# Kernel optimization log

Hardware: AMD Instinct MI355X
Metric: run time of the kernel (lower is better)

The kernel has to match this reference:

```python
import jax, jax.numpy as jnp
import numpy as np

T, B_SZ = 1024, 1024
NX, NU, ND, NM, NDT, NH = 128, 64, 32, 32, 32, 128


def setup_inputs() -> dict:
    key = jax.random.key(0)
    ks = jax.random.split(key, 10)
    return {
        "x": jax.random.normal(ks[0], (B_SZ, NX), jnp.float32),
        "M_flow": jax.random.normal(ks[1], (T, B_SZ, NM), jnp.float32),
        "DT": jax.random.normal(ks[2], (T, B_SZ, NDT), jnp.float32),
        "D": jax.random.normal(ks[3], (T, B_SZ, ND), jnp.float32),
        # ConstrainedLinear(nx, nx): weight and scalar init with torch.rand -> uniform[0,1)
        "A_weight": jax.random.uniform(ks[4], (NX, NX), jnp.float32),
        "A_scalar": jax.random.uniform(ks[5], (NX, NX), jnp.float32),
        # nn.Linear(in, out, bias=False) weights are [out, in]
        "B_w": jax.random.normal(ks[6], (NX, NU), jnp.float32) * (1.0 / np.sqrt(NU)),
        "E_w": jax.random.normal(ks[7], (NX, ND), jnp.float32) * (1.0 / np.sqrt(ND)),
        "hf1_w": jax.random.normal(ks[8], (NH, NM + NDT), jnp.float32) * (1.0 / np.sqrt(NM + NDT)),
        "hf2_w": jax.random.normal(ks[9], (NU, NH), jnp.float32) * (1.0 / np.sqrt(NH)),
    }


def reference(x, M_flow, DT, D, A_weight, A_scalar, B_w, E_w, hf1_w, hf2_w):
    # Constrained weight: ((1 - 0.1*sigmoid(scalar)) * softmax(weight, dim=1)).T
    # It is constant across time, so compute once (torch redundantly recomputes it per step).
    s_clamped = 1.0 - 0.1 * jax.nn.sigmoid(A_scalar)
    W_eff = (s_clamped * jax.nn.softmax(A_weight, axis=1)).T  # [nx, nx]

    # Per-step control input u_t depends only on exogenous M_flow/DT -> vectorize over time.
    md = jnp.concatenate([M_flow, DT], axis=2)                # [T, B, n_m+n_dT]
    h = jax.nn.relu(jnp.einsum('tbi,hi->tbh', md, hf1_w))     # [T, B, n_hidden]
    u = jax.nn.relu(jnp.einsum('tbh,uh->tbu', h, hf2_w))      # [T, B, nu]

    # Precompute additive drive B(u_t) + E(d_t); only x@W_eff is sequential.
    drive = jnp.einsum('tbu,xu->tbx', u, B_w) + jnp.einsum('tbd,xd->tbx', D, E_w)

    def step(x_prev, drive_t):
        x_new = x_prev @ W_eff + drive_t
        return x_new, x_new

    _, X = jax.lax.scan(step, x, drive)  # X: [T, B, nx]
    Y = X[:, :, -1]                      # [T, B]
    return X, Y
```

## Files before the change

### kernel.cpp

```cpp
#include <hip/hip_runtime.h>

typedef _Float16 h4 __attribute__((ext_vector_type(4)));
typedef _Float16 h8 __attribute__((ext_vector_type(8)));
typedef float f4 __attribute__((ext_vector_type(4)));

#define MFMA16(a, b, c) __builtin_amdgcn_mfma_f32_16x16x32_f16((a), (b), (c), 0, 0, 0)

static constexpr int TT  = 1024;
static constexpr int BS  = 1024;
static constexpr int LCH = 32;
static constexpr int NCH = 32;
static constexpr size_t XTOT = (size_t)TT * BS * 128;

static constexpr size_t WS_WT16 = 0;
static constexpr size_t WS_HF1  = 32768;
static constexpr size_t WS_HF2  = 49152;
static constexpr size_t WS_BW   = 65536;
static constexpr size_t WS_EW   = 81920;
static constexpr size_t WS_W32  = 90112;
static constexpr size_t WS_F    = 131072;
static constexpr size_t WS_INIT = WS_F + (size_t)NCH * BS * 128 * 4;
static constexpr size_t WS_DRV  = WS_INIT + (size_t)NCH * BS * 128 * 4;

template <typename T>
__device__ inline T ntload(const T* p) { return __builtin_nontemporal_load(p); }

__global__ void prep_kernel(const float* __restrict__ Aw, const float* __restrict__ As,
                            const float* __restrict__ hf1, const float* __restrict__ hf2,
                            const float* __restrict__ Bw, const float* __restrict__ Ew,
                            char* __restrict__ ws)
{
    const int tid = threadIdx.x;
    const int bid = blockIdx.x;
    if (bid < 128) {
        __shared__ float red[128];
        const int n = bid;
        const float a = Aw[n * 128 + tid];
        red[tid] = a;
        __syncthreads();
        for (int s = 64; s > 0; s >>= 1) {
            if (tid < s) red[tid] = fmaxf(red[tid], red[tid + s]);
            __syncthreads();
        }
        const float mx = red[0];
        __syncthreads();
        const float e = expf(a - mx);
        red[tid] = e;
        __syncthreads();
        for (int s = 64; s > 0; s >>= 1) {
            if (tid < s) red[tid] += red[tid + s];
            __syncthreads();
        }
        const float sm  = e / red[0];
        const float asv = As[n * 128 + tid];
        const float sc  = 1.0f - 0.1f * (1.0f / (1.0f + expf(-asv)));
        ((_Float16*)(ws + WS_WT16))[n * 128 + tid] = (_Float16)(sc * sm);
    } else {
        const int b2 = bid - 128;
        for (int i = b2 * 128 + tid; i < 8192; i += 32 * 128) {
            ((_Float16*)(ws + WS_HF1))[i] = (_Float16)hf1[i];
            ((_Float16*)(ws + WS_HF2))[i] = (_Float16)hf2[i];
            ((_Float16*)(ws + WS_BW))[i]  = (_Float16)Bw[i];
            if (i < 4096) ((_Float16*)(ws + WS_EW))[i] = (_Float16)Ew[i];
        }
    }
}

__global__ void w32_kernel(char* __restrict__ ws)
{
    const int tid  = threadIdx.x;
    const int lane = tid & 63;
    const int w    = tid >> 6;
    const int cl   = lane & 15;
    const int gq   = lane >> 4;

    __shared__ __align__(16) _Float16 Ta[128 * 128];
    __shared__ __align__(16) _Float16 Tb[128 * 128];

    const _Float16* Wt16 = (const _Float16*)(ws + WS_WT16);
    for (int i = tid; i < 2048; i += 256)
        *(h8*)&Ta[i * 8] = *(const h8*)&Wt16[i * 8];
    __syncthreads();

    for (int s = 0; s < 5; ++s) {
        const _Float16* src = (s & 1) ? Tb : Ta;
        _Float16* dst       = (s & 1) ? Ta : Tb;
        f4 acc[8][2];
#pragma unroll
        for (int mt = 0; mt < 8; ++mt)
#pragma unroll
            for (int nt = 0; nt < 2; ++nt) acc[mt][nt] = f4{};
#pragma unroll
        for (int kk = 0; kk < 4; ++kk) {
            h8 b0, b1;
#pragma unroll
            for (int j = 0; j < 8; ++j) {
                const int kr = kk * 32 + gq * 8 + j;
                b0[j] = src[kr * 128 + w * 32 + cl];
                b1[j] = src[kr * 128 + w * 32 + 16 + cl];
            }
#pragma unroll
            for (int mt = 0; mt < 8; ++mt) {
                h8 a = *(const h8*)&src[(mt * 16 + cl) * 128 + kk * 32 + gq * 8];
                acc[mt][0] = MFMA16(a, b0, acc[mt][0]);
                acc[mt][1] = MFMA16(a, b1, acc[mt][1]);
            }
        }
        __syncthreads();
#pragma unroll
        for (int mt = 0; mt < 8; ++mt)
#pragma unroll
            for (int nt = 0; nt < 2; ++nt)
#pragma unroll
                for (int r = 0; r < 4; ++r)
                    dst[(mt * 16 + gq * 4 + r) * 128 + w * 32 + nt * 16 + cl] =
                        (_Float16)acc[mt][nt][r];
        __syncthreads();
    }
    _Float16* W32 = (_Float16*)(ws + WS_W32);
    for (int i = tid; i < 2048; i += 256)
        *(h8*)&W32[i * 8] = *(const h8*)&Tb[i * 8];
}

__global__ __launch_bounds__(256, 4)
void drive_kernel(const float* __restrict__ Mfl, const float* __restrict__ DTi,
                  const float* __restrict__ Din, char* __restrict__ ws)
{
    const int tid  = threadIdx.x;
    const int lane = tid & 63;
    const int w    = tid >> 6;
    const int cl   = lane & 15;
    const int gq   = lane >> 4;
    const int bt   = blockIdx.x & 63;
    const int tq   = blockIdx.x >> 6;
    const int b0   = bt * 16;

    const _Float16* Hf1  = (const _Float16*)(ws + WS_HF1);
    const _Float16* Hf2  = (const _Float16*)(ws + WS_HF2);
    const _Float16* Bw16 = (const _Float16*)(ws + WS_BW);
    const _Float16* Ew16 = (const _Float16*)(ws + WS_EW);
    _Float16* Drv        = (_Float16*)(ws + WS_DRV);

    __shared__ __align__(16) _Float16 mds[4][16 * 64];
    __shared__ __align__(16) _Float16 dts[4][16 * 32];
    __shared__ __align__(16) _Float16 hs[4][16 * 128];
    __shared__ __align__(16) _Float16 us[4][16 * 64];

    const int qrow = (tid & 127) >> 3;
    const int qc4  = (tid & 7) * 4;
    f4 pm[4], pd[4];
#pragma unroll
    for (int s = 0; s < 4; ++s) {
        const size_t t  = (size_t)tq * 4 + s;
        const size_t rb = (t * BS + b0 + qrow) * 32 + qc4;
        pm[s] = (tid < 128) ? ntload((const f4*)&Mfl[rb]) : ntload((const f4*)&DTi[rb]);
        if (tid < 128) pd[s] = ntload((const f4*)&Din[rb]);
    }
#pragma unroll
    for (int s = 0; s < 4; ++s) {
        const int col = (tid < 128) ? qc4 : (32 + qc4);
        h4 hv;
#pragma unroll
        for (int j = 0; j < 4; ++j) hv[j] = (_Float16)pm[s][j];
        *(h4*)&mds[s][qrow * 64 + (((col >> 3) ^ (qrow & 7)) * 8) + (col & 7)] = hv;
        if (tid < 128) {
            h4 h2;
#pragma unroll
            for (int j = 0; j < 4; ++j) h2[j] = (_Float16)pd[s][j];
            *(h4*)&dts[s][qrow * 32 + (((qc4 >> 3) ^ (qrow & 3)) * 8) + (qc4 & 7)] = h2;
        }
    }

    h8 hf1f[2][2], bwf[2][2], ewf[2], hf2f[4];
#pragma unroll
    for (int nt = 0; nt < 2; ++nt) {
        const int ng = w * 32 + nt * 16 + cl;
#pragma unroll
        for (int kk = 0; kk < 2; ++kk) {
            hf1f[nt][kk] = *(const h8*)&Hf1[ng * 64 + kk * 32 + gq * 8];
            bwf[nt][kk]  = *(const h8*)&Bw16[ng * 64 + kk * 32 + gq * 8];
        }
        ewf[nt] = *(const h8*)&Ew16[ng * 32 + gq * 8];
    }
    {
        const int ng = w * 16 + cl;
#pragma unroll
        for (int kk = 0; kk < 4; ++kk)
            hf2f[kk] = *(const h8*)&Hf2[ng * 128 + kk * 32 + gq * 8];
    }
    __syncthreads();

#pragma unroll
    for (int s = 0; s < 4; ++s) {
        f4 ha[2] = {};
#pragma unroll
        for (int kk = 0; kk < 2; ++kk) {
            h8 a = *(const h8*)&mds[s][cl * 64 + (((kk * 4 + gq) ^ (cl & 7)) * 8)];
            ha[0] = MFMA16(hf1f[0][kk], a, ha[0]);
            ha[1] = MFMA16(hf1f[1][kk], a, ha[1]);
        }
#pragma unroll
        for (int nt = 0; nt < 2; ++nt) {
            const int nb8 = w * 4 + nt * 2 + (gq >> 1);
            h4 hv;
#pragma unroll
            for (int r = 0; r < 4; ++r) hv[r] = (_Float16)fmaxf(ha[nt][r], 0.f);
            *(h4*)&hs[s][cl * 128 + ((nb8 ^ cl) & 15) * 8 + (gq & 1) * 4] = hv;
        }
    }
    __syncthreads();

#pragma unroll
    for (int s = 0; s < 4; ++s) {
        f4 ua = {};
#pragma unroll
        for (int kt = 0; kt < 4; ++kt) {
            h8 a = *(const h8*)&hs[s][cl * 128 + (((kt * 4 + gq) ^ cl) & 15) * 8];
            ua = MFMA16(hf2f[kt], a, ua);
        }
        const int nb8 = w * 2 + (gq >> 1);
        h4 hv;
#pragma unroll
        for (int r = 0; r < 4; ++r) hv[r] = (_Float16)fmaxf(ua[r], 0.f);
        *(h4*)&us[s][cl * 64 + ((nb8 ^ (cl & 7)) & 7) * 8 + (gq & 1) * 4] = hv;
    }
    __syncthreads();

#pragma unroll
    for (int s = 0; s < 4; ++s) {
        f4 acc[2] = {};
#pragma unroll
        for (int kk = 0; kk < 2; ++kk) {
            h8 a = *(const h8*)&us[s][cl * 64 + (((kk * 4 + gq) ^ (cl & 7)) & 7) * 8];
            acc[0] = MFMA16(bwf[0][kk], a, acc[0]);
            acc[1] = MFMA16(bwf[1][kk], a, acc[1]);
        }
        {
            h8 a = *(const h8*)&dts[s][cl * 32 + ((gq ^ (cl & 3)) * 8)];
            acc[0] = MFMA16(ewf[0], a, acc[0]);
            acc[1] = MFMA16(ewf[1], a, acc[1]);
        }
        h8 o;
#pragma unroll
        for (int r = 0; r < 4; ++r) { o[r] = (_Float16)acc[0][r]; o[4 + r] = (_Float16)acc[1][r]; }
        const size_t t = (size_t)tq * 4 + s;
        *(h8*)&Drv[((t * 64 + bt) * 256 + tid) * 8] = o;
    }
}

template <bool FINAL>
__global__ __launch_bounds__(256, 2)
void scan_kernel(char* __restrict__ ws,
                 float* __restrict__ Xout, float* __restrict__ Yout)
{
    const int wslot = threadIdx.x >> 6;
    const int wid   = blockIdx.x * 4 + wslot;
    const int lane  = threadIdx.x & 63;
    const int cl = lane & 15, gq = lane >> 4;
    const int c  = wid >> 6;
    const int bt = wid & 63;
    const int b0 = bt * 16;

    const _Float16* Wt16 = (const _Float16*)(ws + WS_WT16);
    const _Float16* Drv  = (const _Float16*)(ws + WS_DRV);
    float* Fbuf       = (float*)(ws + WS_F);
    const float* Init = (const float*)(ws + WS_INIT);

    __shared__ __align__(16) _Float16 tb[4][16 * 128];
    _Float16* tbuf = tb[wslot];

    h8 wf[8][4];
#pragma unroll
    for (int nt = 0; nt < 8; ++nt)
#pragma unroll
        for (int kt = 0; kt < 4; ++kt)
            wf[nt][kt] = *(const h8*)&Wt16[(nt * 16 + cl) * 128 + kt * 32 + gq * 8];

    h8 xf[4];
    if constexpr (FINAL) {
        f4 iv[8];
#pragma unroll
        for (int nt = 0; nt < 8; ++nt)
            iv[nt] = *(const f4*)&Init[((size_t)c * BS + b0 + cl) * 128 + nt * 16 + gq * 4];
#pragma unroll
        for (int nt = 0; nt < 8; ++nt) {
            h4 hv;
#pragma unroll
            for (int r = 0; r < 4; ++r) hv[r] = (_Float16)iv[nt][r];
            *(h4*)&tbuf[cl * 128 + (((nt * 2 + (gq >> 1)) ^ cl) & 15) * 8 + (gq & 1) * 4] = hv;
        }
#pragma unroll
        for (int kt = 0; kt < 4; ++kt)
            xf[kt] = *(const h8*)&tbuf[cl * 128 + (((kt * 4 + gq) ^ cl) & 15) * 8];
    } else {
#pragma unroll
        for (int kt = 0; kt < 4; ++kt) xf[kt] = h8{};
    }

    constexpr size_t STEP = 16384;
    const h8* dp = (const h8*)Drv + (((size_t)(c * LCH) * 64 + bt) * 4) * 64 + lane;
    h8 dra0, dra1, dra2, dra3, drb0, drb1, drb2, drb3;
    dra0 = dp[0];          dra1 = dp[64];          dra2 = dp[128];          dra3 = dp[192];
    drb0 = dp[STEP];       drb1 = dp[STEP + 64];   drb2 = dp[STEP + 128];   drb3 = dp[STEP + 192];

#define SCAN_STEP(K, D0, D1, D2, D3)                                                     \
    {                                                                                    \
        f4 acc[8];                                                                       \
        _Pragma("unroll") for (int r = 0; r < 4; ++r) {                                  \
            acc[0][r] = (float)D0[r]; acc[1][r] = (float)D0[4 + r];                      \
            acc[2][r] = (float)D1[r]; acc[3][r] = (float)D1[4 + r];                      \
            acc[4][r] = (float)D2[r]; acc[5][r] = (float)D2[4 + r];                      \
            acc[6][r] = (float)D3[r]; acc[7][r] = (float)D3[4 + r];                      \
        }                                                                                \
        if ((K) + 2 < LCH) {                                                             \
            D0 = dp[(size_t)((K) + 2) * STEP + 0];                                       \
            D1 = dp[(size_t)((K) + 2) * STEP + 64];                                      \
            D2 = dp[(size_t)((K) + 2) * STEP + 128];                                     \
            D3 = dp[(size_t)((K) + 2) * STEP + 192];                                     \
        }                                                                                \
        _Pragma("unroll") for (int kt = 0; kt < 4; ++kt)                                 \
            _Pragma("unroll") for (int nt = 0; nt < 8; ++nt)                             \
                acc[nt] = MFMA16(wf[nt][kt], xf[kt], acc[nt]);                           \
        if constexpr (FINAL) {                                                           \
            const size_t t = (size_t)c * LCH + (K);                                      \
            float* xp = &Xout[(t * BS + b0 + cl) * 128 + gq * 4];                        \
            _Pragma("unroll") for (int nt = 0; nt < 8; ++nt)                             \
                __builtin_nontemporal_store(acc[nt], (f4*)&xp[nt * 16]);                 \
            if (gq == 3)                                                                 \
                __builtin_nontemporal_store(acc[7][3], &Yout[t * BS + b0 + cl]);         \
        } else if ((K) == LCH - 1) {                                                     \
            _Pragma("unroll") for (int nt = 0; nt < 8; ++nt)                             \
                *(f4*)&Fbuf[((size_t)c * BS + b0 + cl) * 128 + nt * 16 + gq * 4] =       \
                    acc[nt];                                                             \
        }                                                                                \
        if ((K) < LCH - 1) {                                                             \
            _Pragma("unroll") for (int nt = 0; nt < 8; ++nt) {                           \
                h4 hv;                                                                   \
                _Pragma("unroll") for (int r = 0; r < 4; ++r)                            \
                    hv[r] = (_Float16)acc[nt][r];                                        \
                *(h4*)&tbuf[cl * 128 + (((nt * 2 + (gq >> 1)) ^ cl) & 15) * 8 +          \
                            (gq & 1) * 4] = hv;                                          \
            }                                                                            \
            _Pragma("unroll") for (int kt = 0; kt < 4; ++kt)                             \
                xf[kt] = *(const h8*)&tbuf[cl * 128 + (((kt * 4 + gq) ^ cl) & 15) * 8];  \
        }                                                                                \
    }

    for (int k = 0; k < LCH; k += 2) {
        SCAN_STEP(k, dra0, dra1, dra2, dra3);
        SCAN_STEP(k + 1, drb0, drb1, drb2, drb3);
    }
#undef SCAN_STEP
}

__global__ __launch_bounds__(64, 1)
void carry_kernel(const float* __restrict__ x0, char* __restrict__ ws, int n_steps)
{
    const int lane = threadIdx.x;
    const int cl = lane & 15, gq = lane >> 4;
    const int b0 = blockIdx.x * 16;

    const _Float16* W32 = (const _Float16*)(ws + WS_W32);
    const float* Fbuf   = (const float*)(ws + WS_F);
    float* Init         = (float*)(ws + WS_INIT);

    __shared__ __align__(16) _Float16 tbuf[16 * 128];

    h8 wf[8][4];
#pragma unroll
    for (int nt = 0; nt < 8; ++nt)
#pragma unroll
        for (int kt = 0; kt < 4; ++kt)
            wf[nt][kt] = *(const h8*)&W32[(nt * 16 + cl) * 128 + kt * 32 + gq * 8];

    h8 xf[4];
    {
        f4 iv[8];
#pragma unroll
        for (int nt = 0; nt < 8; ++nt)
            iv[nt] = *(const f4*)&x0[(size_t)(b0 + cl) * 128 + nt * 16 + gq * 4];
#pragma unroll
        for (int nt = 0; nt < 8; ++nt)
            *(f4*)&Init[(size_t)(b0 + cl) * 128 + nt * 16 + gq * 4] = iv[nt];
#pragma unroll
        for (int nt = 0; nt < 8; ++nt) {
            h4 hv;
#pragma unroll
            for (int r = 0; r < 4; ++r) hv[r] = (_Float16)iv[nt][r];
            *(h4*)&tbuf[cl * 128 + (((nt * 2 + (gq >> 1)) ^ cl) & 15) * 8 + (gq & 1) * 4] = hv;
        }
#pragma unroll
        for (int kt = 0; kt < 4; ++kt)
            xf[kt] = *(const h8*)&tbuf[cl * 128 + (((kt * 4 + gq) ^ cl) & 15) * 8];
    }

    for (int cc = 1; cc <= n_steps; ++cc) {
        f4 acc[8];
#pragma unroll
        for (int nt = 0; nt < 8; ++nt)
            acc[nt] = *(const f4*)&Fbuf[((size_t)(cc - 1) * BS + b0 + cl) * 128 + nt * 16 + gq * 4];
#pragma unroll
        for (int kt = 0; kt < 4; ++kt)
#pragma unroll
            for (int nt = 0; nt < 8; ++nt)
                acc[nt] = MFMA16(wf[nt][kt], xf[kt], acc[nt]);
#pragma unroll
        for (int nt = 0; nt < 8; ++nt)
            *(f4*)&Init[((size_t)cc * BS + b0 + cl) * 128 + nt * 16 + gq * 4] = acc[nt];
        if (cc < n_steps) {
#pragma unroll
            for (int nt = 0; nt < 8; ++nt) {
                h4 hv;
#pragma unroll
                for (int r = 0; r < 4; ++r) hv[r] = (_Float16)acc[nt][r];
                *(h4*)&tbuf[cl * 128 + (((nt * 2 + (gq >> 1)) ^ cl) & 15) * 8 + (gq & 1) * 4] = hv;
            }
#pragma unroll
            for (int kt = 0; kt < 4; ++kt)
                xf[kt] = *(const h8*)&tbuf[cl * 128 + (((kt * 4 + gq) ^ cl) & 15) * 8];
        }
    }
}

extern "C" void kernel_launch(void* const* d_in, const int* in_sizes, int n_in,
                              void* d_out, int out_size, void* d_ws, size_t ws_size,
                              hipStream_t stream)
{
    const float* x_in = (const float*)d_in[0];
    const float* Mfl  = (const float*)d_in[1];
    const float* DTi  = (const float*)d_in[2];
    const float* Din  = (const float*)d_in[3];
    const float* Aw   = (const float*)d_in[4];
    const float* As   = (const float*)d_in[5];
    const float* Bw   = (const float*)d_in[6];
    const float* Ew   = (const float*)d_in[7];
    const float* hf1  = (const float*)d_in[8];
    const float* hf2  = (const float*)d_in[9];
    char* ws    = (char*)d_ws;
    float* Xout = (float*)d_out;
    float* Yout = Xout + XTOT;

    prep_kernel<<<dim3(160), dim3(128), 0, stream>>>(Aw, As, hf1, hf2, Bw, Ew, ws);
    w32_kernel<<<dim3(1), dim3(256), 0, stream>>>(ws);

    drive_kernel<<<dim3(256 * 64), dim3(256), 0, stream>>>(Mfl, DTi, Din, ws);
    scan_kernel<false><<<dim3(496), dim3(256), 0, stream>>>(ws, nullptr, nullptr);
    carry_kernel<<<dim3(64), dim3(64), 0, stream>>>(x_in, ws, 31);
    scan_kernel<true><<<dim3(512), dim3(256), 0, stream>>>(ws, Xout, Yout);
}
```

Baseline: 456.0 us.

## Fuse drive computation with local chunk scan and split pipeline into halves

Replaces the separate drive kernel and the non-final scan pass with a fused kernel that computes the MLP drive per step and immediately runs the zero-initialised local chunk scan, writing drive and chunk-end states. The timeline is split into two halves of 16 chunks, each with its own fused, carry and final-scan launches, so the drive buffer only needs to hold half the time range. The w32 matrix power kernel is also restructured to keep both the matrix and its transpose in padded shared memory, avoiding strided scalar loads. This removes one full read of the drive buffer. In exchange, the fused kernel runs only 256 blocks at one block per CU, and the halves are serialised, which may lower parallelism.

```diff
diff --git a/kernel.cpp b/kernel.cpp
--- a/kernel.cpp
+++ b/kernel.cpp
@@ -73,198 +73,263 @@
     const int w    = tid >> 6;
     const int cl   = lane & 15;
     const int gq   = lane >> 4;
-
-    __shared__ __align__(16) _Float16 Ta[128 * 128];
-    __shared__ __align__(16) _Float16 Tb[128 * 128];
+    constexpr int LDP = 136;
+
+    __shared__ __align__(16) _Float16 G[2][128 * LDP];
+    __shared__ __align__(16) _Float16 H[2][128 * LDP];
 
     const _Float16* Wt16 = (const _Float16*)(ws + WS_WT16);
     for (int i = tid; i < 2048; i += 256)
-        *(h8*)&Ta[i * 8] = *(const h8*)&Wt16[i * 8];
+        *(h8*)&G[0][(i >> 4) * LDP + (i & 15) * 8] = *(const h8*)&Wt16[i * 8];
     __syncthreads();
-
+    for (int i = tid; i < 16384; i += 256) {
+        const int r = i >> 7, cc = i & 127;
+        H[0][cc * LDP + r] = G[0][r * LDP + cc];
+    }
+    __syncthreads();
+
+    int cur = 0;
     for (int s = 0; s < 5; ++s) {
-        const _Float16* src = (s & 1) ? Tb : Ta;
-        _Float16* dst       = (s & 1) ? Ta : Tb;
-        f4 acc[8][2];
+        const _Float16* Gs = G[cur];
+        const _Float16* Hs = H[cur];
+        _Float16* Gd = G[cur ^ 1];
+        _Float16* Hd = H[cur ^ 1];
+        f4 aG[8][2], aH[8][2];
 #pragma unroll
         for (int mt = 0; mt < 8; ++mt)
 #pragma unroll
-            for (int nt = 0; nt < 2; ++nt) acc[mt][nt] = f4{};
+            for (int nt = 0; nt < 2; ++nt) { aG[mt][nt] = f4{}; aH[mt][nt] = f4{}; }
 #pragma unroll
         for (int kk = 0; kk < 4; ++kk) {
-            h8 b0, b1;
-#pragma unroll
-            for (int j = 0; j < 8; ++j) {
-                const int kr = kk * 32 + gq * 8 + j;
-                b0[j] = src[kr * 128 + w * 32 + cl];
-                b1[j] = src[kr * 128 + w * 32 + 16 + cl];
+            h8 bG0 = *(const h8*)&Hs[((w * 2 + 0) * 16 + cl) * LDP + kk * 32 + gq * 8];
+            h8 bG1 = *(const h8*)&Hs[((w * 2 + 1) * 16 + cl) * LDP + kk * 32 + gq * 8];
+            h8 bH0 = *(const h8*)&Gs[((w * 2 + 0) * 16 + cl) * LDP + kk * 32 + gq * 8];
+            h8 bH1 = *(const h8*)&Gs[((w * 2 + 1) * 16 + cl) * LDP + kk * 32 + gq * 8];
+#pragma unroll
+            for (int mt = 0; mt < 8; ++mt) {
+                h8 ag = *(const h8*)&Gs[(mt * 16 + cl) * LDP + kk * 32 + gq * 8];
+                h8 ah = *(const h8*)&Hs[(mt * 16 + cl) * LDP + kk * 32 + gq * 8];
+                aG[mt][0] = MFMA16(ag, bG0, aG[mt][0]);
+                aG[mt][1] = MFMA16(ag, bG1, aG[mt][1]);
+                aH[mt][0] = MFMA16(ah, bH0, aH[mt][0]);
+                aH[mt][1] = MFMA16(ah, bH1, aH[mt][1]);
             }
-#pragma unroll
-            for (int mt = 0; mt < 8; ++mt) {
-                h8 a = *(const h8*)&src[(mt * 16 + cl) * 128 + kk * 32 + gq * 8];
-                acc[mt][0] = MFMA16(a, b0, acc[mt][0]);
-                acc[mt][1] = MFMA16(a, b1, acc[mt][1]);
+        }
+#pragma unroll
+        for (int mt = 0; mt < 8; ++mt)
+#pragma unroll
+            for (int nt = 0; nt < 2; ++nt) {
+                h4 hg, hh;
+#pragma unroll
+                for (int r = 0; r < 4; ++r) {
+                    hg[r] = (_Float16)aG[mt][nt][r];
+                    hh[r] = (_Float16)aH[mt][nt][r];
+                }
+                const int col  = (w * 2 + nt) * 16 + cl;
+                const int rowb = mt * 16 + gq * 4;
+                *(h4*)&Hd[col * LDP + rowb] = hg;
+                *(h4*)&Gd[col * LDP + rowb] = hh;
             }
-        }
         __syncthreads();
-#pragma unroll
-        for (int mt = 0; mt < 8; ++mt)
-#pragma unroll
-            for (int nt = 0; nt < 2; ++nt)
-#pragma unroll
-                for (int r = 0; r < 4; ++r)
-                    dst[(mt * 16 + gq * 4 + r) * 128 + w * 32 + nt * 16 + cl] =
-                        (_Float16)acc[mt][nt][r];
-        __syncthreads();
+        cur ^= 1;
     }
     _Float16* W32 = (_Float16*)(ws + WS_W32);
     for (int i = tid; i < 2048; i += 256)
-        *(h8*)&W32[i * 8] = *(const h8*)&Tb[i * 8];
+        *(h8*)&W32[i * 8] = *(const h8*)&G[cur][(i >> 4) * LDP + (i & 15) * 8];
 }
 
-__global__ __launch_bounds__(256, 4)
-void drive_kernel(const float* __restrict__ Mfl, const float* __restrict__ DTi,
-                  const float* __restrict__ Din, char* __restrict__ ws)
+__global__ __launch_bounds__(256, 1)
+void fused_local(const float* __restrict__ Mfl, const float* __restrict__ DTi,
+                 const float* __restrict__ Din, char* __restrict__ ws, int c0)
 {
-    const int tid  = threadIdx.x;
-    const int lane = tid & 63;
-    const int w    = tid >> 6;
-    const int cl   = lane & 15;
-    const int gq   = lane >> 4;
-    const int bt   = blockIdx.x & 63;
-    const int tq   = blockIdx.x >> 6;
-    const int b0   = bt * 16;
-
-    const _Float16* Hf1  = (const _Float16*)(ws + WS_HF1);
-    const _Float16* Hf2  = (const _Float16*)(ws + WS_HF2);
-    const _Float16* Bw16 = (const _Float16*)(ws + WS_BW);
-    const _Float16* Ew16 = (const _Float16*)(ws + WS_EW);
-    _Float16* Drv        = (_Float16*)(ws + WS_DRV);
-
-    __shared__ __align__(16) _Float16 mds[4][16 * 64];
-    __shared__ __align__(16) _Float16 dts[4][16 * 32];
-    __shared__ __align__(16) _Float16 hs[4][16 * 128];
-    __shared__ __align__(16) _Float16 us[4][16 * 64];
-
-    const int qrow = (tid & 127) >> 3;
-    const int qc4  = (tid & 7) * 4;
-    f4 pm[4], pd[4];
-#pragma unroll
-    for (int s = 0; s < 4; ++s) {
-        const size_t t  = (size_t)tq * 4 + s;
-        const size_t rb = (t * BS + b0 + qrow) * 32 + qc4;
-        pm[s] = (tid < 128) ? ntload((const f4*)&Mfl[rb]) : ntload((const f4*)&DTi[rb]);
-        if (tid < 128) pd[s] = ntload((const f4*)&Din[rb]);
-    }
-#pragma unroll
-    for (int s = 0; s < 4; ++s) {
-        const int col = (tid < 128) ? qc4 : (32 + qc4);
-        h4 hv;
-#pragma unroll
-        for (int j = 0; j < 4; ++j) hv[j] = (_Float16)pm[s][j];
-        *(h4*)&mds[s][qrow * 64 + (((col >> 3) ^ (qrow & 7)) * 8) + (col & 7)] = hv;
-        if (tid < 128) {
-            h4 h2;
-#pragma unroll
-            for (int j = 0; j < 4; ++j) h2[j] = (_Float16)pd[s][j];
-            *(h4*)&dts[s][qrow * 32 + (((qc4 >> 3) ^ (qrow & 3)) * 8) + (qc4 & 7)] = h2;
-        }
-    }
-
-    h8 hf1f[2][2], bwf[2][2], ewf[2], hf2f[4];
-#pragma unroll
-    for (int nt = 0; nt < 2; ++nt) {
-        const int ng = w * 32 + nt * 16 + cl;
-#pragma unroll
-        for (int kk = 0; kk < 2; ++kk) {
-            hf1f[nt][kk] = *(const h8*)&Hf1[ng * 64 + kk * 32 + gq * 8];
-            bwf[nt][kk]  = *(const h8*)&Bw16[ng * 64 + kk * 32 + gq * 8];
-        }
-        ewf[nt] = *(const h8*)&Ew16[ng * 32 + gq * 8];
-    }
+    const int tid   = threadIdx.x;
+    const int wslot = tid >> 6;
+    const int lane  = tid & 63;
+    const int cl = lane & 15, gq = lane >> 4;
+    const int wid = blockIdx.x * 4 + wslot;
+    const int c   = c0 + (wid >> 6);
+    const int bt  = wid & 63;
+    const int b0  = bt * 16;
+
+    __shared__ __align__(16) _Float16 Lhf1[128 * 64];
+    __shared__ __align__(16) _Float16 Lhf2[64 * 128];
+    __shared__ __align__(16) _Float16 Lbw[128 * 64];
+    __shared__ __align__(16) _Float16 Lew[128 * 32];
+    __shared__ __align__(16) _Float16 tb[4][16 * 128];
+
     {
-        const int ng = w * 16 + cl;
-#pragma unroll
-        for (int kk = 0; kk < 4; ++kk)
-            hf2f[kk] = *(const h8*)&Hf2[ng * 128 + kk * 32 + gq * 8];
-    }
+        const h8* g1 = (const h8*)(ws + WS_HF1);
+        const h8* g2 = (const h8*)(ws + WS_HF2);
+        const h8* gb = (const h8*)(ws + WS_BW);
+        const h8* ge = (const h8*)(ws + WS_EW);
+        for (int i = tid; i < 1024; i += 256) {
+            const int r = i >> 3, c8 = i & 7;
+            *(h8*)&Lhf1[(r * 8 + (c8 ^ (r & 7))) * 8] = g1[i];
+            *(h8*)&Lbw[(r * 8 + (c8 ^ (r & 7))) * 8]  = gb[i];
+        }
+        for (int i = tid; i < 1024; i += 256) {
+            const int r = i >> 4, c8 = i & 15;
+            *(h8*)&Lhf2[(r * 16 + (c8 ^ (r & 15))) * 8] = g2[i];
+        }
+        for (int i = tid; i < 512; i += 256) {
+            const int r = i >> 2, c8 = i & 3;
+            *(h8*)&Lew[(r * 4 + (c8 ^ (r & 3))) * 8] = ge[i];
+        }
+    }
+
+    const _Float16* Wt16 = (const _Float16*)(ws + WS_WT16);
+    h8 wf[8][4];
+#pragma unroll
+    for (int nt = 0; nt < 8; ++nt)
+#pragma unroll
+        for (int kt = 0; kt < 4; ++kt)
+            wf[nt][kt] = *(const h8*)&Wt16[(nt * 16 + cl) * 128 + kt * 32 + gq * 8];
     __syncthreads();
 
-#pragma unroll
-    for (int s = 0; s < 4; ++s) {
-        f4 ha[2] = {};
-#pragma unroll
-        for (int kk = 0; kk < 2; ++kk) {
-            h8 a = *(const h8*)&mds[s][cl * 64 + (((kk * 4 + gq) ^ (cl & 7)) * 8)];
-            ha[0] = MFMA16(hf1f[0][kk], a, ha[0]);
-            ha[1] = MFMA16(hf1f[1][kk], a, ha[1]);
-        }
-#pragma unroll
-        for (int nt = 0; nt < 2; ++nt) {
-            const int nb8 = w * 4 + nt * 2 + (gq >> 1);
+    _Float16* tbuf = tb[wslot];
+    _Float16* Drv  = (_Float16*)(ws + WS_DRV);
+    float* Fbuf    = (float*)(ws + WS_F);
+
+    h8 xf[4];
+#pragma unroll
+    for (int kt = 0; kt < 4; ++kt) xf[kt] = h8{};
+
+    f4 Lm0, Lm1, Lt0, Lt1, Ld0, Ld1;
+    auto ILOAD = [&](int k) {
+        const size_t t  = (size_t)c * LCH + k;
+        const size_t ba = (t * BS + b0 + cl) * 32 + gq * 8;
+        Lm0 = ntload((const f4*)&Mfl[ba]);
+        Lm1 = ntload((const f4*)&Mfl[ba + 4]);
+        Lt0 = ntload((const f4*)&DTi[ba]);
+        Lt1 = ntload((const f4*)&DTi[ba + 4]);
+        Ld0 = ntload((const f4*)&Din[ba]);
+        Ld1 = ntload((const f4*)&Din[ba + 4]);
+    };
+    h8 fm, fdt, fd;
+    auto ICVT = [&]() {
+#pragma unroll
+        for (int j = 0; j < 4; ++j) {
+            fm[j] = (_Float16)Lm0[j];  fm[4 + j] = (_Float16)Lm1[j];
+            fdt[j] = (_Float16)Lt0[j]; fdt[4 + j] = (_Float16)Lt1[j];
+            fd[j] = (_Float16)Ld0[j];  fd[4 + j] = (_Float16)Ld1[j];
+        }
+    };
+    ILOAD(0);
+    ICVT();
+
+    for (int k = 0; k < LCH; ++k) {
+        f4 ah[8];
+#pragma unroll
+        for (int nt = 0; nt < 8; ++nt) {
+            f4 z = {};
+            h8 a0 = *(const h8*)&Lhf1[((nt * 16 + cl) * 8 + (gq ^ (cl & 7))) * 8];
+            h8 a1 = *(const h8*)&Lhf1[((nt * 16 + cl) * 8 + ((4 + gq) ^ (cl & 7))) * 8];
+            ah[nt] = MFMA16(a0, fm, z);
+            ah[nt] = MFMA16(a1, fdt, ah[nt]);
+        }
+#pragma unroll
+        for (int nt = 0; nt < 8; ++nt) {
             h4 hv;
 #pragma unroll
-            for (int r = 0; r < 4; ++r) hv[r] = (_Float16)fmaxf(ha[nt][r], 0.f);
-            *(h4*)&hs[s][cl * 128 + ((nb8 ^ cl) & 15) * 8 + (gq & 1) * 4] = hv;
-        }
-    }
-    __syncthreads();
-
-#pragma unroll
-    for (int s = 0; s < 4; ++s) {
-        f4 ua = {};
-#pragma unroll
-        for (int kt = 0; kt < 4; ++kt) {
-            h8 a = *(const h8*)&hs[s][cl * 128 + (((kt * 4 + gq) ^ cl) & 15) * 8];
-            ua = MFMA16(hf2f[kt], a, ua);
-        }
-        const int nb8 = w * 2 + (gq >> 1);
-        h4 hv;
-#pragma unroll
-        for (int r = 0; r < 4; ++r) hv[r] = (_Float16)fmaxf(ua[r], 0.f);
-        *(h4*)&us[s][cl * 64 + ((nb8 ^ (cl & 7)) & 7) * 8 + (gq & 1) * 4] = hv;
-    }
-    __syncthreads();
-
-#pragma unroll
-    for (int s = 0; s < 4; ++s) {
-        f4 acc[2] = {};
-#pragma unroll
-        for (int kk = 0; kk < 2; ++kk) {
-            h8 a = *(const h8*)&us[s][cl * 64 + (((kk * 4 + gq) ^ (cl & 7)) & 7) * 8];
-            acc[0] = MFMA16(bwf[0][kk], a, acc[0]);
-            acc[1] = MFMA16(bwf[1][kk], a, acc[1]);
-        }
+            for (int r = 0; r < 4; ++r) hv[r] = (_Float16)fmaxf(ah[nt][r], 0.f);
+            *(h4*)&tbuf[cl * 128 + (((nt * 2 + (gq >> 1)) ^ cl) & 15) * 8 + (gq & 1) * 4] = hv;
+        }
+        h8 hfr[4];
+#pragma unroll
+        for (int kt = 0; kt < 4; ++kt)
+            hfr[kt] = *(const h8*)&tbuf[cl * 128 + (((kt * 4 + gq) ^ cl) & 15) * 8];
+
+        f4 au[4];
+#pragma unroll
+        for (int nt = 0; nt < 4; ++nt) {
+            f4 z = {};
+            au[nt] = z;
+#pragma unroll
+            for (int kt = 0; kt < 4; ++kt) {
+                h8 a = *(const h8*)&Lhf2[((nt * 16 + cl) * 16 + ((kt * 4 + gq) ^ cl)) * 8];
+                au[nt] = MFMA16(a, hfr[kt], au[nt]);
+            }
+        }
+#pragma unroll
+        for (int nt = 0; nt < 4; ++nt) {
+            h4 uv;
+#pragma unroll
+            for (int r = 0; r < 4; ++r) uv[r] = (_Float16)fmaxf(au[nt][r], 0.f);
+            const int ub8 = nt * 2 + (gq >> 1);
+            *(h4*)&tbuf[cl * 128 + ((ub8 ^ (cl & 7)) & 7) * 8 + (gq & 1) * 4] = uv;
+        }
+        h8 ufr0 = *(const h8*)&tbuf[cl * 128 + ((gq ^ (cl & 7)) & 7) * 8];
+        h8 ufr1 = *(const h8*)&tbuf[cl * 128 + (((4 + gq) ^ (cl & 7)) & 7) * 8];
+
+        f4 acc[8];
+#pragma unroll
+        for (int nt = 0; nt < 8; ++nt) {
+            f4 z = {};
+            h8 b0w = *(const h8*)&Lbw[((nt * 16 + cl) * 8 + (gq ^ (cl & 7))) * 8];
+            h8 b1w = *(const h8*)&Lbw[((nt * 16 + cl) * 8 + ((4 + gq) ^ (cl & 7))) * 8];
+            h8 ewf = *(const h8*)&Lew[((nt * 16 + cl) * 4 + (gq ^ (cl & 3))) * 8];
+            acc[nt] = MFMA16(b0w, ufr0, z);
+            acc[nt] = MFMA16(b1w, ufr1, acc[nt]);
+            acc[nt] = MFMA16(ewf, fd, acc[nt]);
+        }
+
         {
-            h8 a = *(const h8*)&dts[s][cl * 32 + ((gq ^ (cl & 3)) * 8)];
-            acc[0] = MFMA16(ewf[0], a, acc[0]);
-            acc[1] = MFMA16(ewf[1], a, acc[1]);
-        }
-        h8 o;
-#pragma unroll
-        for (int r = 0; r < 4; ++r) { o[r] = (_Float16)acc[0][r]; o[4 + r] = (_Float16)acc[1][r]; }
-        const size_t t = (size_t)tq * 4 + s;
-        *(h8*)&Drv[((t * 64 + bt) * 256 + tid) * 8] = o;
+            const size_t tl = (size_t)(c - c0) * LCH + k;
+#pragma unroll
+            for (int p = 0; p < 4; ++p) {
+                h8 o;
+#pragma unroll
+                for (int r = 0; r < 4; ++r) {
+                    o[r]     = (_Float16)acc[2 * p][r];
+                    o[4 + r] = (_Float16)acc[2 * p + 1][r];
+                }
+                *(h8*)&Drv[(((tl * 64 + bt) * 4 + p) * 64 + lane) * 8] = o;
+            }
+        }
+
+        if (k + 1 < LCH) ILOAD(k + 1);
+
+#pragma unroll
+        for (int kt = 0; kt < 4; ++kt)
+#pragma unroll
+            for (int nt = 0; nt < 8; ++nt)
+                acc[nt] = MFMA16(wf[nt][kt], xf[kt], acc[nt]);
+
+        if (k == LCH - 1) {
+#pragma unroll
+            for (int nt = 0; nt < 8; ++nt)
+                *(f4*)&Fbuf[((size_t)c * BS + b0 + cl) * 128 + nt * 16 + gq * 4] = acc[nt];
+        } else {
+#pragma unroll
+            for (int nt = 0; nt < 8; ++nt) {
+                h4 hv;
+#pragma unroll
+                for (int r = 0; r < 4; ++r) hv[r] = (_Float16)acc[nt][r];
+                *(h4*)&tbuf[cl * 128 + (((nt * 2 + (gq >> 1)) ^ cl) & 15) * 8 + (gq & 1) * 4] = hv;
+            }
+#pragma unroll
+            for (int kt = 0; kt < 4; ++kt)
+                xf[kt] = *(const h8*)&tbuf[cl * 128 + (((kt * 4 + gq) ^ cl) & 15) * 8];
+            ICVT();
+        }
     }
 }
 
-template <bool FINAL>
 __global__ __launch_bounds__(256, 2)
-void scan_kernel(char* __restrict__ ws,
-                 float* __restrict__ Xout, float* __restrict__ Yout)
+void scan_final(char* __restrict__ ws, int c0,
+                float* __restrict__ Xout, float* __restrict__ Yout)
 {
     const int wslot = threadIdx.x >> 6;
     const int wid   = blockIdx.x * 4 + wslot;
     const int lane  = threadIdx.x & 63;
     const int cl = lane & 15, gq = lane >> 4;
-    const int c  = wid >> 6;
+    const int c  = c0 + (wid >> 6);
     const int bt = wid & 63;
     const int b0 = bt * 16;
 
     const _Float16* Wt16 = (const _Float16*)(ws + WS_WT16);
     const _Float16* Drv  = (const _Float16*)(ws + WS_DRV);
-    float* Fbuf       = (float*)(ws + WS_F);
-    const float* Init = (const float*)(ws + WS_INIT);
+    const float* Init    = (const float*)(ws + WS_INIT);
 
     __shared__ __align__(16) _Float16 tb[4][16 * 128];
     _Float16* tbuf = tb[wslot];
@@ -277,7 +342,7 @@
             wf[nt][kt] = *(const h8*)&Wt16[(nt * 16 + cl) * 128 + kt * 32 + gq * 8];
 
     h8 xf[4];
-    if constexpr (FINAL) {
+    {
         f4 iv[8];
 #pragma unroll
         for (int nt = 0; nt < 8; ++nt)
@@ -292,16 +357,13 @@
 #pragma unroll
         for (int kt = 0; kt < 4; ++kt)
             xf[kt] = *(const h8*)&tbuf[cl * 128 + (((kt * 4 + gq) ^ cl) & 15) * 8];
-    } else {
-#pragma unroll
-        for (int kt = 0; kt < 4; ++kt) xf[kt] = h8{};
     }
 
     constexpr size_t STEP = 16384;
-    const h8* dp = (const h8*)Drv + (((size_t)(c * LCH) * 64 + bt) * 4) * 64 + lane;
+    const h8* dp = (const h8*)Drv + (((size_t)((c - c0) * LCH) * 64 + bt) * 4) * 64 + lane;
     h8 dra0, dra1, dra2, dra3, drb0, drb1, drb2, drb3;
-    dra0 = dp[0];          dra1 = dp[64];          dra2 = dp[128];          dra3 = dp[192];
-    drb0 = dp[STEP];       drb1 = dp[STEP + 64];   drb2 = dp[STEP + 128];   drb3 = dp[STEP + 192];
+    dra0 = dp[0];    dra1 = dp[64];        dra2 = dp[128];        dra3 = dp[192];
+    drb0 = dp[STEP]; drb1 = dp[STEP + 64]; drb2 = dp[STEP + 128]; drb3 = dp[STEP + 192];
 
 #define SCAN_STEP(K, D0, D1, D2, D3)                                                     \
     {                                                                                    \
@@ -321,17 +383,13 @@
         _Pragma("unroll") for (int kt = 0; kt < 4; ++kt)                                 \
             _Pragma("unroll") for (int nt = 0; nt < 8; ++nt)                             \
                 acc[nt] = MFMA16(wf[nt][kt], xf[kt], acc[nt]);                           \
-        if constexpr (FINAL) {                                                           \
+        {                                                                                \
             const size_t t = (size_t)c * LCH + (K);                                      \
             float* xp = &Xout[(t * BS + b0 + cl) * 128 + gq * 4];                        \
             _Pragma("unroll") for (int nt = 0; nt < 8; ++nt)                             \
                 __builtin_nontemporal_store(acc[nt], (f4*)&xp[nt * 16]);                 \
             if (gq == 3)                                                                 \
                 __builtin_nontemporal_store(acc[7][3], &Yout[t * BS + b0 + cl]);         \
-        } else if ((K) == LCH - 1) {                                                     \
-            _Pragma("unroll") for (int nt = 0; nt < 8; ++nt)                             \
-                *(f4*)&Fbuf[((size_t)c * BS + b0 + cl) * 128 + nt * 16 + gq * 4] =       \
-                    acc[nt];                                                             \
         }                                                                                \
         if ((K) < LCH - 1) {                                                             \
             _Pragma("unroll") for (int nt = 0; nt < 8; ++nt) {                           \
@@ -354,7 +412,8 @@
 }
 
 __global__ __launch_bounds__(64, 1)
-void carry_kernel(const float* __restrict__ x0, char* __restrict__ ws, int n_steps)
+void carry_kernel(const float* __restrict__ x0, char* __restrict__ ws,
+                  int cc_lo, int n_steps, int copy0)
 {
     const int lane = threadIdx.x;
     const int cl = lane & 15, gq = lane >> 4;
@@ -379,9 +438,11 @@
 #pragma unroll
         for (int nt = 0; nt < 8; ++nt)
             iv[nt] = *(const f4*)&x0[(size_t)(b0 + cl) * 128 + nt * 16 + gq * 4];
-#pragma unroll
-        for (int nt = 0; nt < 8; ++nt)
-            *(f4*)&Init[(size_t)(b0 + cl) * 128 + nt * 16 + gq * 4] = iv[nt];
+        if (copy0) {
+#pragma unroll
+            for (int nt = 0; nt < 8; ++nt)
+                *(f4*)&Init[((size_t)cc_lo * BS + b0 + cl) * 128 + nt * 16 + gq * 4] = iv[nt];
+        }
 #pragma unroll
         for (int nt = 0; nt < 8; ++nt) {
             h4 hv;
@@ -394,7 +455,8 @@
             xf[kt] = *(const h8*)&tbuf[cl * 128 + (((kt * 4 + gq) ^ cl) & 15) * 8];
     }
 
-    for (int cc = 1; cc <= n_steps; ++cc) {
+    for (int i = 1; i <= n_steps; ++i) {
+        const int cc = cc_lo + i;
         f4 acc[8];
 #pragma unroll
         for (int nt = 0; nt < 8; ++nt)
@@ -407,7 +469,7 @@
 #pragma unroll
         for (int nt = 0; nt < 8; ++nt)
             *(f4*)&Init[((size_t)cc * BS + b0 + cl) * 128 + nt * 16 + gq * 4] = acc[nt];
-        if (cc < n_steps) {
+        if (i < n_steps) {
 #pragma unroll
             for (int nt = 0; nt < 8; ++nt) {
                 h4 hv;
@@ -439,12 +501,16 @@
     char* ws    = (char*)d_ws;
     float* Xout = (float*)d_out;
     float* Yout = Xout + XTOT;
+    const float* Init16 = (const float*)(ws + WS_INIT) + (size_t)16 * BS * 128;
 
     prep_kernel<<<dim3(160), dim3(128), 0, stream>>>(Aw, As, hf1, hf2, Bw, Ew, ws);
     w32_kernel<<<dim3(1), dim3(256), 0, stream>>>(ws);
 
-    drive_kernel<<<dim3(256 * 64), dim3(256), 0, stream>>>(Mfl, DTi, Din, ws);
-    scan_kernel<false><<<dim3(496), dim3(256), 0, stream>>>(ws, nullptr, nullptr);
-    carry_kernel<<<dim3(64), dim3(64), 0, stream>>>(x_in, ws, 31);
-    scan_kernel<true><<<dim3(512), dim3(256), 0, stream>>>(ws, Xout, Yout);
+    fused_local<<<dim3(256), dim3(256), 0, stream>>>(Mfl, DTi, Din, ws, 0);
+    carry_kernel<<<dim3(64), dim3(64), 0, stream>>>(x_in, ws, 0, 16, 1);
+    scan_final<<<dim3(256), dim3(256), 0, stream>>>(ws, 0, Xout, Yout);
+
+    fused_local<<<dim3(256), dim3(256), 0, stream>>>(Mfl, DTi, Din, ws, 16);
+    carry_kernel<<<dim3(64), dim3(64), 0, stream>>>(Init16, ws, 16, 15, 0);
+    scan_final<<<dim3(256), dim3(256), 0, stream>>>(ws, 16, Xout, Yout);
 }
```

Measured after the change: 517.6 us. 13.5% more time.
